# Performance work log

Measured on AMD Instinct MI355X. Metric: run time of the kernel, lower is better.

The kernel has to match this reference:

```python
import jax, jax.numpy as jnp
import numpy as np

B, S, D_IN, D, H = 2, 2048, 512, 1024, 16
HD = D // H


def _linear_params(key, d_in, d_out):
    kw, kb = jax.random.split(key)
    bound = 1.0 / np.sqrt(d_in)
    W = jax.random.uniform(kw, (d_in, d_out), jnp.float32, -bound, bound)
    b = jax.random.uniform(kb, (d_out,), jnp.float32, -bound, bound)
    return W, b


def setup_inputs() -> dict:
    key = jax.random.key(0)
    keys = jax.random.split(key, 8)
    x = jax.random.normal(keys[0], (B, S, D_IN), jnp.float32)
    We, be = _linear_params(keys[1], D_IN, D)
    Wq, bq = _linear_params(keys[2], D, D)
    Wk, bk = _linear_params(keys[3], D, D)
    Wv, bv = _linear_params(keys[4], D, D)
    W0, b0 = _linear_params(keys[5], D, D)
    W1, b1 = _linear_params(keys[6], D, D)
    W2, b2 = _linear_params(keys[7], D, D)
    return {"x": x, "We": We, "be": be, "Wq": Wq, "bq": bq, "Wk": Wk, "bk": bk,
            "Wv": Wv, "bv": bv, "W0": W0, "b0": b0, "W1": W1, "b1": b1, "W2": W2, "b2": b2}


def reference(x, We, be, Wq, bq, Wk, bk, Wv, bv, W0, b0, W1, b1, W2, b2):
    # embedding
    e = x @ We + be                                   # [B,S,D]
    q = (e @ Wq + bq).reshape(B, S, H, HD)            # [B,S,H,hd]
    k = (e @ Wk + bk).reshape(B, S, H, HD)
    v = (e @ Wv + bv).reshape(B, S, H, HD)
    scale = 1.0 / jnp.sqrt(jnp.float32(HD))
    scores = jnp.einsum('bqhd,bkhd->bhqk', q, k) * scale
    attn = jax.nn.softmax(scores, axis=-1)            # [B,H,S,S]
    ctx = jnp.einsum('bhqk,bkhd->bqhd', attn, v).reshape(B, S, D)
    mha = e + (ctx @ W0 + b0)                         # residual
    ffn = jax.nn.relu(mha @ W1 + b1) @ W2 + b2
    return mha + ffn
```

## Files before the change

### kernel.cpp

```cpp
#include <hip/hip_runtime.h>

typedef unsigned short u16;
typedef __bf16 bf16x8 __attribute__((ext_vector_type(8)));
typedef float f32x4 __attribute__((ext_vector_type(4)));

__device__ __forceinline__ float bf2f(u16 u) {
  return __builtin_bit_cast(float, (unsigned)u << 16);
}
__device__ __forceinline__ u16 f2bf(float f) {
  unsigned u = __builtin_bit_cast(unsigned, f);
  u += 0x7FFFu + ((u >> 16) & 1u);
  return (u16)(u >> 16);
}
__device__ __forceinline__ unsigned pk2(float a, float b) {
  return (unsigned)f2bf(a) | ((unsigned)f2bf(b) << 16);
}
__device__ __forceinline__ unsigned pk2t(float a, float b) {
  return __builtin_amdgcn_perm(__builtin_bit_cast(unsigned, b),
                               __builtin_bit_cast(unsigned, a), 0x07060302u);
}
__device__ __forceinline__ f32x4 mfma16(bf16x8 a, bf16x8 b, f32x4 c) {
  return __builtin_amdgcn_mfma_f32_16x16x32_bf16(a, b, c, 0, 0, 0);
}
__device__ __forceinline__ void async_cp16(const u16* g, u16* l) {
  __builtin_amdgcn_global_load_lds((const __attribute__((address_space(1))) void*)g,
                                   (__attribute__((address_space(3))) void*)l, 16, 0, 0);
}
#define S_BARRIER() asm volatile("s_barrier" ::: "memory")

#define TSP 72
__global__ __launch_bounds__(256) void prep_fused(
    const float* __restrict__ We, const float* __restrict__ Wq,
    const float* __restrict__ Wk, const float* __restrict__ Wv,
    const float* __restrict__ W0, const float* __restrict__ W1,
    const float* __restrict__ W2, const float* __restrict__ x,
    const float* __restrict__ bq, const float* __restrict__ bk,
    const float* __restrict__ bv, u16* Wet, u16* qkvWt, u16* W0t, u16* W1t,
    u16* W2t, u16* xb, float* biasqkv) {
  const int z = blockIdx.z;
  const int tid = threadIdx.x;
  if (z >= 7) {
    if (z == 15) {
      int i = (blockIdx.y * 16 + blockIdx.x) * 256 + tid;
      if (i < 3072)
        biasqkv[i] = i < 1024 ? bq[i] : (i < 2048 ? bk[i - 1024] : bv[i - 2048]);
      return;
    }
    int blin = (z - 7) * 256 + blockIdx.y * 16 + blockIdx.x;
    int idx = (blin * 256 + tid) * 4;
    float4 f = *(const float4*)&x[idx];
    ushort4 o;
    o.x = f2bf(f.x); o.y = f2bf(f.y); o.z = f2bf(f.z); o.w = f2bf(f.w);
    *(ushort4*)&xb[idx] = o;
    return;
  }
  const float* in;
  u16* out;
  int out_rs = 1024;
  if (z == 0) { if (blockIdx.y >= 8) return; in = We; out = Wet; out_rs = 512; }
  else if (z == 1) { in = Wq; out = qkvWt; }
  else if (z == 2) { in = Wk; out = qkvWt + 1048576; }
  else if (z == 3) { in = Wv; out = qkvWt + 2097152; }
  else if (z == 4) { in = W0; out = W0t; }
  else if (z == 5) { in = W1; out = W1t; }
  else { in = W2; out = W2t; }
  __shared__ alignas(16) u16 T[64][TSP];
  const int r0 = blockIdx.y * 64, c0 = blockIdx.x * 64;
#pragma unroll
  for (int it = 0; it < 4; ++it) {
    int vi = it * 256 + tid;
    int i = vi >> 4, j4 = (vi & 15) * 4;
    float4 f = *(const float4*)&in[(size_t)(r0 + i) * 1024 + c0 + j4];
    T[i][j4 + 0] = f2bf(f.x);
    T[i][j4 + 1] = f2bf(f.y);
    T[i][j4 + 2] = f2bf(f.z);
    T[i][j4 + 3] = f2bf(f.w);
  }
  __syncthreads();
#pragma unroll
  for (int it = 0; it < 2; ++it) {
    int vi = it * 256 + tid;
    int i = vi >> 3, j8 = (vi & 7) * 8;
    bf16x8 v;
#pragma unroll
    for (int u = 0; u < 8; ++u) ((u16*)&v)[u] = T[j8 + u][i];
    *(bf16x8*)&out[(size_t)(c0 + i) * out_rs + r0 + j8] = v;
  }
}

template <int TM, int TN>
__global__ __launch_bounds__(256, (TM == 128 && TN == 128) ? 2
                                  : (TM == 128)            ? 3
                                                           : 5) void gemm_mfma(
    const u16* __restrict__ A, const u16* __restrict__ Bt,
    const float* __restrict__ bias, const u16* __restrict__ res,
    void* __restrict__ Cout, int M, int N, int K, int relu, int f32out) {
  constexpr int MT = TM / 32;
  constexpr int NT = TN / 32;
  constexpr int AI = TM / 32;
  constexpr int BI = TN / 32;
  __shared__ alignas(16) u16 As[2][TM * 64];
  __shared__ alignas(16) u16 Bs[2][TN * 64];
  const int tid = threadIdx.x;
  const int wave = tid >> 6, lane = tid & 63;
  const int quad = lane >> 4, l16 = lane & 15;
  const int ib = blockIdx.x;
  int by, bx;
  if constexpr (TM == 128) { by = (ib & 7) * 4 + ((ib >> 3) & 3); bx = ib >> 5; }
  else { by = (ib & 7) * 8 + ((ib >> 3) & 7); bx = ib >> 6; }
  const int m0 = by * TM, n0 = bx * TN;
  const int wm = (wave & 1) * (TM / 2), wn = (wave >> 1) * (TN / 2);

  f32x4 acc[MT][NT];
#pragma unroll
  for (int i = 0; i < MT; ++i)
#pragma unroll
    for (int j = 0; j < NT; ++j) acc[i][j] = (f32x4){0.f, 0.f, 0.f, 0.f};

  const int srow = lane >> 3;
  const int schunk = (lane & 7) ^ (srow & 7);
  const u16* Ag = A + (size_t)(m0 + wave * (TM / 4) + srow) * K + schunk * 8;
  const u16* Bg = Bt + (size_t)(n0 + wave * (TN / 4) + srow) * K + schunk * 8;
  u16* AsW0 = &As[0][wave * (TM / 4) * 64];
  u16* BsW0 = &Bs[0][wave * (TN / 4) * 64];
  u16* AsW1 = &As[1][wave * (TM / 4) * 64];
  u16* BsW1 = &Bs[1][wave * (TN / 4) * 64];

#define GEMM_ISSUE(ab, bb, k)                                     \
  {                                                               \
    _Pragma("unroll") for (int i = 0; i < AI; ++i)                \
        async_cp16(Ag + (k) + (size_t)i * 8 * K, (ab) + i * 512); \
    _Pragma("unroll") for (int i = 0; i < BI; ++i)                \
        async_cp16(Bg + (k) + (size_t)i * 8 * K, (bb) + i * 512); \
  }

  GEMM_ISSUE(AsW0, BsW0, 0);
  const int T = K >> 6;
  const int swz = (l16 & 7);
  for (int t = 0; t < T; ++t) {
    const int cb = t & 1;
    S_BARRIER();
    const int kn = (t + 1 < T) ? ((t + 1) << 6) : 0;
    if (cb == 0) GEMM_ISSUE(AsW1, BsW1, kn) else GEMM_ISSUE(AsW0, BsW0, kn);
    if constexpr (AI + BI == 8)
      asm volatile("s_waitcnt vmcnt(8)" ::: "memory");
    else if constexpr (AI + BI == 6)
      asm volatile("s_waitcnt vmcnt(6)" ::: "memory");
    else
      asm volatile("s_waitcnt vmcnt(4)" ::: "memory");
    S_BARRIER();
#pragma unroll
    for (int kk = 0; kk < 2; ++kk) {
      bf16x8 af[MT], bfr[NT];
#pragma unroll
      for (int mt = 0; mt < MT; ++mt)
        af[mt] = *(const bf16x8*)&As[cb][(wm + mt * 16 + l16) * 64 +
                                        ((kk * 4 + quad) ^ swz) * 8];
#pragma unroll
      for (int nt = 0; nt < NT; ++nt)
        bfr[nt] = *(const bf16x8*)&Bs[cb][(wn + nt * 16 + l16) * 64 +
                                          ((kk * 4 + quad) ^ swz) * 8];
#pragma unroll
      for (int mt = 0; mt < MT; ++mt)
#pragma unroll
        for (int nt = 0; nt < NT; ++nt)
          acc[mt][nt] = mfma16(af[mt], bfr[nt], acc[mt][nt]);
    }
  }
  asm volatile("s_waitcnt vmcnt(0)" ::: "memory");

#pragma unroll
  for (int nt = 0; nt < NT; ++nt) {
    int col = n0 + wn + nt * 16 + l16;
    float bv = bias[col];
#pragma unroll
    for (int mt = 0; mt < MT; ++mt) {
#pragma unroll
      for (int r = 0; r < 4; ++r) {
        int row = m0 + wm + mt * 16 + quad * 4 + r;
        float v = acc[mt][nt][r] + bv;
        if (res) v += bf2f(res[(size_t)row * N + col]);
        if (relu) v = fmaxf(v, 0.f);
        if (f32out)
          ((float*)Cout)[(size_t)row * N + col] = v;
        else
          ((u16*)Cout)[(size_t)row * N + col] = f2bf(v);
      }
    }
  }
}

__global__ __launch_bounds__(256, 2) void attn_kernel(
    const u16* __restrict__ QKV, const u16* __restrict__ Vt,
    u16* __restrict__ O) {
  __shared__ alignas(16) u16 Ks[2][64 * 64];
  __shared__ alignas(16) u16 Vs[2][64 * 64];
  __shared__ alignas(16) u16 Ps[4][32 * 64];
  const int tid = threadIdx.x;
  const int wave = tid >> 6, lane = tid & 63;
  const int quad = lane >> 4, l16 = lane & 15;
  const int ib = blockIdx.x;
  const int bh = ib & 31, b = bh >> 4, h = bh & 15;
  const int q0 = (ib >> 5) * 128 + wave * 32;

  bf16x8 qf[2][2];
#pragma unroll
  for (int qt = 0; qt < 2; ++qt) {
    const size_t qoff = (size_t)(b * 2048 + q0 + qt * 16 + l16) * 3072 + h * 64;
#pragma unroll
    for (int kk = 0; kk < 2; ++kk) {
      bf16x8 raw = *(const bf16x8*)&QKV[qoff + kk * 32 + quad * 8];
#pragma unroll
      for (int u = 0; u < 8; ++u)
        ((u16*)&raw)[u] = f2bf(0.125f * bf2f(((u16*)&raw)[u]));
      qf[qt][kk] = raw;
    }
  }
  bf16x8 ones;
#pragma unroll
  for (int u = 0; u < 8; ++u) ((u16*)&ones)[u] = 0x3F80;

  f32x4 o[4][2];
  f32x4 l_acc[2] = {(f32x4){0.f, 0.f, 0.f, 0.f}, (f32x4){0.f, 0.f, 0.f, 0.f}};
#pragma unroll
  for (int mt = 0; mt < 4; ++mt)
#pragma unroll
    for (int qt = 0; qt < 2; ++qt) o[mt][qt] = (f32x4){0.f, 0.f, 0.f, 0.f};

  const int srow = lane >> 3;
  const int schunk = (lane & 7) ^ (srow & 7);
  const u16* Kg = QKV + (size_t)(b * 2048 + wave * 16 + srow) * 3072 + 1024 +
                  h * 64 + schunk * 8;
  const u16* Vg = Vt + (size_t)((b * 16 + h) * 64 + wave * 16 + srow) * 2048 +
                  schunk * 8;
  u16* KsW0 = &Ks[0][(wave * 16) * 64];
  u16* VsW0 = &Vs[0][(wave * 16) * 64];
  u16* KsW1 = &Ks[1][(wave * 16) * 64];
  u16* VsW1 = &Vs[1][(wave * 16) * 64];

#define ATTN_ISSUE(kb, vb, kt)                                \
  {                                                           \
    async_cp16(Kg + (size_t)(kt) * 3072, (kb));               \
    async_cp16(Kg + (size_t)((kt) + 8) * 3072, (kb) + 512);   \
    async_cp16(Vg + (kt), (vb));                              \
    async_cp16(Vg + (kt) + (size_t)8 * 2048, (vb) + 512);     \
  }

  ATTN_ISSUE(KsW0, VsW0, 0);
  const int swz = (l16 & 7);
  u16* PsW = &Ps[wave][0];
  for (int t = 0; t < 32; ++t) {
    const int cb = t & 1;
    S_BARRIER();
    const int ktn = (t + 1 < 32) ? ((t + 1) * 64) : 0;
    if (cb == 0) ATTN_ISSUE(KsW1, VsW1, ktn) else ATTN_ISSUE(KsW0, VsW0, ktn);
    asm volatile("s_waitcnt vmcnt(4)" ::: "memory");
    S_BARRIER();

    f32x4 st[4][2];
#pragma unroll
    for (int km = 0; km < 4; ++km)
#pragma unroll
      for (int qt = 0; qt < 2; ++qt) st[km][qt] = (f32x4){0.f, 0.f, 0.f, 0.f};
    __builtin_amdgcn_s_setprio(1);
#pragma unroll
    for (int kk = 0; kk < 2; ++kk)
#pragma unroll
      for (int km = 0; km < 4; ++km) {
        bf16x8 kf = *(const bf16x8*)&Ks[cb][(km * 16 + l16) * 64 +
                                           ((kk * 4 + quad) ^ swz) * 8];
        st[km][0] = mfma16(kf, qf[0][kk], st[km][0]);
        st[km][1] = mfma16(kf, qf[1][kk], st[km][1]);
      }
    __builtin_amdgcn_s_setprio(0);

#pragma unroll
    for (int qt = 0; qt < 2; ++qt)
#pragma unroll
      for (int km = 0; km < 4; ++km) {
        float e0 = __expf(st[km][qt][0]), e1 = __expf(st[km][qt][1]);
        float e2 = __expf(st[km][qt][2]), e3 = __expf(st[km][qt][3]);
        uint2 pk;
        pk.x = pk2t(e0, e1);
        pk.y = pk2t(e2, e3);
        *(uint2*)&PsW[(qt * 16 + l16) * 64 +
                      ((km * 2 + (quad >> 1)) ^ swz) * 8 + (quad & 1) * 4] = pk;
      }
    asm volatile("s_waitcnt lgkmcnt(0)" ::: "memory");

    __builtin_amdgcn_s_setprio(1);
#pragma unroll
    for (int kk2 = 0; kk2 < 2; ++kk2) {
      bf16x8 pf0 =
          *(const bf16x8*)&PsW[l16 * 64 + ((kk2 * 4 + quad) ^ swz) * 8];
      bf16x8 pf1 = *(const bf16x8*)&PsW[(16 + l16) * 64 +
                                        ((kk2 * 4 + quad) ^ swz) * 8];
      l_acc[0] = mfma16(ones, pf0, l_acc[0]);
      l_acc[1] = mfma16(ones, pf1, l_acc[1]);
#pragma unroll
      for (int mt = 0; mt < 4; ++mt) {
        bf16x8 vf = *(const bf16x8*)&Vs[cb][(mt * 16 + l16) * 64 +
                                           ((kk2 * 4 + quad) ^ swz) * 8];
        o[mt][0] = mfma16(vf, pf0, o[mt][0]);
        o[mt][1] = mfma16(vf, pf1, o[mt][1]);
      }
    }
    __builtin_amdgcn_s_setprio(0);
  }
  asm volatile("s_waitcnt vmcnt(0)" ::: "memory");

#pragma unroll
  for (int qt = 0; qt < 2; ++qt) {
    float inv = 1.f / l_acc[qt][0];
    size_t base = (size_t)(b * 2048 + q0 + qt * 16 + l16) * 1024 + h * 64;
#pragma unroll
    for (int mt = 0; mt < 4; ++mt) {
      uint2 pk;
      pk.x = pk2(o[mt][qt][0] * inv, o[mt][qt][1] * inv);
      pk.y = pk2(o[mt][qt][2] * inv, o[mt][qt][3] * inv);
      *(uint2*)&O[base + mt * 16 + quad * 4] = pk;
    }
  }
}

__global__ __launch_bounds__(256) void transpose_v(const u16* __restrict__ QKV,
                                                   u16* __restrict__ vt) {
  const int bh = blockIdx.y;
  const int b = bh >> 4, h = bh & 15;
  const int s0 = blockIdx.x * 64;
  const u16* in = QKV + (size_t)b * 2048 * 3072 + 2048 + h * 64;
  u16* out = vt + (size_t)bh * 131072;
  __shared__ alignas(16) u16 T[64][TSP];
  const int tid = threadIdx.x;
#pragma unroll
  for (int it = 0; it < 2; ++it) {
    int vi = it * 256 + tid;
    int i = vi >> 3, j8 = (vi & 7) * 8;
    *(bf16x8*)&T[i][j8] = *(const bf16x8*)&in[(size_t)(s0 + i) * 3072 + j8];
  }
  __syncthreads();
#pragma unroll
  for (int it = 0; it < 2; ++it) {
    int vi = it * 256 + tid;
    int i = vi >> 3, j8 = (vi & 7) * 8;
    bf16x8 vv;
#pragma unroll
    for (int u = 0; u < 8; ++u) ((u16*)&vv)[u] = T[j8 + u][i];
    *(bf16x8*)&out[(size_t)i * 2048 + s0 + j8] = vv;
  }
}

extern "C" void kernel_launch(void* const* d_in, const int* in_sizes, int n_in,
                              void* d_out, int out_size, void* d_ws,
                              size_t ws_size, hipStream_t stream) {
  const float* x = (const float*)d_in[0];
  const float* We = (const float*)d_in[1];
  const float* be = (const float*)d_in[2];
  const float* Wq = (const float*)d_in[3];
  const float* bq = (const float*)d_in[4];
  const float* Wk = (const float*)d_in[5];
  const float* bk = (const float*)d_in[6];
  const float* Wv = (const float*)d_in[7];
  const float* bv = (const float*)d_in[8];
  const float* W0 = (const float*)d_in[9];
  const float* b0 = (const float*)d_in[10];
  const float* W1 = (const float*)d_in[11];
  const float* b1 = (const float*)d_in[12];
  const float* W2 = (const float*)d_in[13];
  const float* b2 = (const float*)d_in[14];

  u16* ws = (u16*)d_ws;
  u16* xb = ws;
  u16* Wet = xb + 2097152;
  u16* qkvWt = Wet + 524288;
  u16* ctx = ws;
  u16* W0t = qkvWt + 3145728;
  u16* W1t = W0t + 1048576;
  u16* W2t = W1t + 1048576;
  float* biasqkv = (float*)(W2t + 1048576);
  u16* e = W2t + 1048576 + 6144;
  u16* qkv = e + 4194304;
  u16* vtb = qkv + 12582912;
  u16* mha = qkv;
  u16* h1 = e;

  prep_fused<<<dim3(16, 16, 16), 256, 0, stream>>>(
      We, Wq, Wk, Wv, W0, W1, W2, x, bq, bk, bv, Wet, qkvWt, W0t, W1t, W2t,
      xb, biasqkv);

  gemm_mfma<64, 64><<<1024, 256, 0, stream>>>(xb, Wet, be, nullptr, e, 4096,
                                              1024, 512, 0, 0);
  gemm_mfma<128, 128><<<768, 256, 0, stream>>>(e, qkvWt, biasqkv, nullptr, qkv,
                                               4096, 3072, 1024, 0, 0);
  transpose_v<<<dim3(32, 32), 256, 0, stream>>>(qkv, vtb);
  attn_kernel<<<512, 256, 0, stream>>>(qkv, vtb, ctx);
  gemm_mfma<64, 64><<<1024, 256, 0, stream>>>(ctx, W0t, b0, e, mha, 4096, 1024,
                                              1024, 0, 0);
  gemm_mfma<64, 64><<<1024, 256, 0, stream>>>(mha, W1t, b1, nullptr, h1, 4096,
                                              1024, 1024, 1, 0);
  gemm_mfma<64, 64><<<1024, 256, 0, stream>>>(h1, W2t, b2, mha, d_out, 4096,
                                              1024, 1024, 0, 1);
}
```

Baseline: 261.8 us.

## Fold embedding weights into QKV projection to shrink the QKV GEMM's K dimension

Precomputes the combined weight Wc = We·Wqkv (a 3072x512 GEMM over the weights) and the combined bias bc = be·Wqkv + bqkv, so QKV is computed directly from x with K=512 instead of from e with K=1024. This roughly halves the FLOPs of the largest projection, at the cost of an extra small weight GEMM, a bias kernel and a bf16 copy of We written during prep. The extra bf16 rounding of the combined weights slightly changes numerics. The QKV GEMM now uses 128x64 tiles, and the 8-load wait path is removed.

Result: slower. 283.9 us (+8.4%).

```diff
diff --git a/kernel.cpp b/kernel.cpp
--- a/kernel.cpp
+++ b/kernel.cpp
@@ -36,7 +36,7 @@
     const float* __restrict__ W2, const float* __restrict__ x,
     const float* __restrict__ bq, const float* __restrict__ bk,
     const float* __restrict__ bv, u16* Wet, u16* qkvWt, u16* W0t, u16* W1t,
-    u16* W2t, u16* xb, float* biasqkv) {
+    u16* W2t, u16* xb, float* biasqkv, u16* Web) {
   const int z = blockIdx.z;
   const int tid = threadIdx.x;
   if (z >= 7) {
@@ -71,10 +71,14 @@
     int vi = it * 256 + tid;
     int i = vi >> 4, j4 = (vi & 15) * 4;
     float4 f = *(const float4*)&in[(size_t)(r0 + i) * 1024 + c0 + j4];
-    T[i][j4 + 0] = f2bf(f.x);
-    T[i][j4 + 1] = f2bf(f.y);
-    T[i][j4 + 2] = f2bf(f.z);
-    T[i][j4 + 3] = f2bf(f.w);
+    ushort4 o;
+    o.x = f2bf(f.x); o.y = f2bf(f.y); o.z = f2bf(f.z); o.w = f2bf(f.w);
+    T[i][j4 + 0] = o.x;
+    T[i][j4 + 1] = o.y;
+    T[i][j4 + 2] = o.z;
+    T[i][j4 + 3] = o.w;
+    if (z == 0)
+      *(ushort4*)&Web[(size_t)(r0 + i) * 1024 + c0 + j4] = o;
   }
   __syncthreads();
 #pragma unroll
@@ -88,10 +92,24 @@
   }
 }
 
-template <int TM, int TN>
-__global__ __launch_bounds__(256, (TM == 128 && TN == 128) ? 2
-                                  : (TM == 128)            ? 3
-                                                           : 5) void gemm_mfma(
+__global__ __launch_bounds__(256) void bc_kernel(const u16* __restrict__ qkvWt,
+                                                 const float* __restrict__ be,
+                                                 const float* __restrict__ biasqkv,
+                                                 float* __restrict__ bc) {
+  int n = blockIdx.x * 256 + threadIdx.x;
+  if (n >= 3072) return;
+  const u16* row = qkvWt + (size_t)n * 1024;
+  float s = biasqkv[n];
+  for (int j = 0; j < 1024; j += 8) {
+    bf16x8 v = *(const bf16x8*)&row[j];
+#pragma unroll
+    for (int u = 0; u < 8; ++u) s += be[j + u] * bf2f(((u16*)&v)[u]);
+  }
+  bc[n] = s;
+}
+
+template <int TM, int TN, bool SWZ = true>
+__global__ __launch_bounds__(256, (TM == 128) ? 3 : 5) void gemm_mfma(
     const u16* __restrict__ A, const u16* __restrict__ Bt,
     const float* __restrict__ bias, const u16* __restrict__ res,
     void* __restrict__ Cout, int M, int N, int K, int relu, int f32out) {
@@ -106,7 +124,8 @@
   const int quad = lane >> 4, l16 = lane & 15;
   const int ib = blockIdx.x;
   int by, bx;
-  if constexpr (TM == 128) { by = (ib & 7) * 4 + ((ib >> 3) & 3); bx = ib >> 5; }
+  if constexpr (!SWZ) { const int yb = M / TM; by = ib % yb; bx = ib / yb; }
+  else if constexpr (TM == 128) { by = (ib & 7) * 4 + ((ib >> 3) & 3); bx = ib >> 5; }
   else { by = (ib & 7) * 8 + ((ib >> 3) & 7); bx = ib >> 6; }
   const int m0 = by * TM, n0 = bx * TN;
   const int wm = (wave & 1) * (TM / 2), wn = (wave >> 1) * (TN / 2);
@@ -142,9 +161,7 @@
     S_BARRIER();
     const int kn = (t + 1 < T) ? ((t + 1) << 6) : 0;
     if (cb == 0) GEMM_ISSUE(AsW1, BsW1, kn) else GEMM_ISSUE(AsW0, BsW0, kn);
-    if constexpr (AI + BI == 8)
-      asm volatile("s_waitcnt vmcnt(8)" ::: "memory");
-    else if constexpr (AI + BI == 6)
+    if constexpr (AI + BI == 6)
       asm volatile("s_waitcnt vmcnt(6)" ::: "memory");
     else
       asm volatile("s_waitcnt vmcnt(4)" ::: "memory");
@@ -172,7 +189,7 @@
 #pragma unroll
   for (int nt = 0; nt < NT; ++nt) {
     int col = n0 + wn + nt * 16 + l16;
-    float bv = bias[col];
+    float bv = bias ? bias[col] : 0.f;
 #pragma unroll
     for (int mt = 0; mt < MT; ++mt) {
 #pragma unroll
@@ -383,15 +400,21 @@
   u16* vtb = qkv + 12582912;
   u16* mha = qkv;
   u16* h1 = e;
+  u16* Web = e;
+  u16* Wct = vtb;
+  float* bc = (float*)(vtb + 4194304);
 
   prep_fused<<<dim3(16, 16, 16), 256, 0, stream>>>(
       We, Wq, Wk, Wv, W0, W1, W2, x, bq, bk, bv, Wet, qkvWt, W0t, W1t, W2t,
-      xb, biasqkv);
-
+      xb, biasqkv, Web);
+
+  bc_kernel<<<12, 256, 0, stream>>>(qkvWt, be, biasqkv, bc);
+  gemm_mfma<64, 64, false><<<384, 256, 0, stream>>>(
+      qkvWt, Web, nullptr, nullptr, Wct, 3072, 512, 1024, 0, 0);
+  gemm_mfma<128, 64><<<1536, 256, 0, stream>>>(xb, Wct, bc, nullptr, qkv, 4096,
+                                               3072, 512, 0, 0);
   gemm_mfma<64, 64><<<1024, 256, 0, stream>>>(xb, Wet, be, nullptr, e, 4096,
                                               1024, 512, 0, 0);
-  gemm_mfma<128, 128><<<768, 256, 0, stream>>>(e, qkvWt, biasqkv, nullptr, qkv,
-                                               4096, 3072, 1024, 0, 0);
   transpose_v<<<dim3(32, 32), 256, 0, stream>>>(qkv, vtb);
   attn_kernel<<<512, 256, 0, stream>>>(qkv, vtb, ctx);
   gemm_mfma<64, 64><<<1024, 256, 0, stream>>>(ctx, W0t, b0, e, mha, 4096, 1024,
```

## Fuse V transpose into QKV GEMM epilogue and switch to 128x64 tiles

Applied to the files above, without the earlier changes.

The QKV projection GEMM now writes the V third of its output directly in transposed per-head layout, so the separate transpose_v kernel launch and its extra read/write of V are removed. The QKV GEMM tile changes from 128x128 to 128x64 with 1536 blocks, which gives more blocks but less reuse per block. The transposed stores are 4-element strided writes along the sequence dimension, which may coalesce poorly.

Result: faster. 249.2 us, median of 4 (-4.8%).

```diff
diff --git a/kernel.cpp b/kernel.cpp
--- a/kernel.cpp
+++ b/kernel.cpp
@@ -88,13 +88,12 @@
   }
 }
 
-template <int TM, int TN>
-__global__ __launch_bounds__(256, (TM == 128 && TN == 128) ? 2
-                                  : (TM == 128)            ? 3
-                                                           : 5) void gemm_mfma(
+template <int TM, int TN, bool VT = false>
+__global__ __launch_bounds__(256, (TM == 128) ? 3 : 5) void gemm_mfma(
     const u16* __restrict__ A, const u16* __restrict__ Bt,
     const float* __restrict__ bias, const u16* __restrict__ res,
-    void* __restrict__ Cout, int M, int N, int K, int relu, int f32out) {
+    void* __restrict__ Cout, int M, int N, int K, int relu, int f32out,
+    u16* __restrict__ vt) {
   constexpr int MT = TM / 32;
   constexpr int NT = TN / 32;
   constexpr int AI = TM / 32;
@@ -142,9 +141,7 @@
     S_BARRIER();
     const int kn = (t + 1 < T) ? ((t + 1) << 6) : 0;
     if (cb == 0) GEMM_ISSUE(AsW1, BsW1, kn) else GEMM_ISSUE(AsW0, BsW0, kn);
-    if constexpr (AI + BI == 8)
-      asm volatile("s_waitcnt vmcnt(8)" ::: "memory");
-    else if constexpr (AI + BI == 6)
+    if constexpr (AI + BI == 6)
       asm volatile("s_waitcnt vmcnt(6)" ::: "memory");
     else
       asm volatile("s_waitcnt vmcnt(4)" ::: "memory");
@@ -172,19 +169,33 @@
 #pragma unroll
   for (int nt = 0; nt < NT; ++nt) {
     int col = n0 + wn + nt * 16 + l16;
-    float bv = bias[col];
+    float bv = bias ? bias[col] : 0.f;
 #pragma unroll
     for (int mt = 0; mt < MT; ++mt) {
+      int row0 = m0 + wm + mt * 16 + quad * 4;
+      float vv[4];
 #pragma unroll
       for (int r = 0; r < 4; ++r) {
-        int row = m0 + wm + mt * 16 + quad * 4 + r;
         float v = acc[mt][nt][r] + bv;
-        if (res) v += bf2f(res[(size_t)row * N + col]);
+        if (res) v += bf2f(res[(size_t)(row0 + r) * N + col]);
         if (relu) v = fmaxf(v, 0.f);
-        if (f32out)
-          ((float*)Cout)[(size_t)row * N + col] = v;
-        else
-          ((u16*)Cout)[(size_t)row * N + col] = f2bf(v);
+        vv[r] = v;
+      }
+      if (VT && col >= 2048) {
+        int bb = row0 >> 11, ss = row0 & 2047;
+        int hh = (col >> 6) & 15, dd = col & 63;
+        uint2 pk;
+        pk.x = pk2(vv[0], vv[1]);
+        pk.y = pk2(vv[2], vv[3]);
+        *(uint2*)&vt[(((size_t)(bb * 16 + hh) * 64 + dd) << 11) + ss] = pk;
+      } else {
+#pragma unroll
+        for (int r = 0; r < 4; ++r) {
+          if (f32out)
+            ((float*)Cout)[(size_t)(row0 + r) * N + col] = vv[r];
+          else
+            ((u16*)Cout)[(size_t)(row0 + r) * N + col] = f2bf(vv[r]);
+        }
       }
     }
   }
@@ -320,33 +331,6 @@
       pk.y = pk2(o[mt][qt][2] * inv, o[mt][qt][3] * inv);
       *(uint2*)&O[base + mt * 16 + quad * 4] = pk;
     }
-  }
-}
-
-__global__ __launch_bounds__(256) void transpose_v(const u16* __restrict__ QKV,
-                                                   u16* __restrict__ vt) {
-  const int bh = blockIdx.y;
-  const int b = bh >> 4, h = bh & 15;
-  const int s0 = blockIdx.x * 64;
-  const u16* in = QKV + (size_t)b * 2048 * 3072 + 2048 + h * 64;
-  u16* out = vt + (size_t)bh * 131072;
-  __shared__ alignas(16) u16 T[64][TSP];
-  const int tid = threadIdx.x;
-#pragma unroll
-  for (int it = 0; it < 2; ++it) {
-    int vi = it * 256 + tid;
-    int i = vi >> 3, j8 = (vi & 7) * 8;
-    *(bf16x8*)&T[i][j8] = *(const bf16x8*)&in[(size_t)(s0 + i) * 3072 + j8];
-  }
-  __syncthreads();
-#pragma unroll
-  for (int it = 0; it < 2; ++it) {
-    int vi = it * 256 + tid;
-    int i = vi >> 3, j8 = (vi & 7) * 8;
-    bf16x8 vv;
-#pragma unroll
-    for (int u = 0; u < 8; ++u) ((u16*)&vv)[u] = T[j8 + u][i];
-    *(bf16x8*)&out[(size_t)i * 2048 + s0 + j8] = vv;
   }
 }
 
@@ -389,15 +373,14 @@
       xb, biasqkv);
 
   gemm_mfma<64, 64><<<1024, 256, 0, stream>>>(xb, Wet, be, nullptr, e, 4096,
-                                              1024, 512, 0, 0);
-  gemm_mfma<128, 128><<<768, 256, 0, stream>>>(e, qkvWt, biasqkv, nullptr, qkv,
-                                               4096, 3072, 1024, 0, 0);
-  transpose_v<<<dim3(32, 32), 256, 0, stream>>>(qkv, vtb);
+                                              1024, 512, 0, 0, nullptr);
+  gemm_mfma<128, 64, true><<<1536, 256, 0, stream>>>(
+      e, qkvWt, biasqkv, nullptr, qkv, 4096, 3072, 1024, 0, 0, vtb);
   attn_kernel<<<512, 256, 0, stream>>>(qkv, vtb, ctx);
   gemm_mfma<64, 64><<<1024, 256, 0, stream>>>(ctx, W0t, b0, e, mha, 4096, 1024,
-                                              1024, 0, 0);
+                                              1024, 0, 0, nullptr);
   gemm_mfma<64, 64><<<1024, 256, 0, stream>>>(mha, W1t, b1, nullptr, h1, 4096,
-                                              1024, 1024, 1, 0);
+                                              1024, 1024, 1, 0, nullptr);
   gemm_mfma<64, 64><<<1024, 256, 0, stream>>>(h1, W2t, b2, mha, d_out, 4096,
-                                              1024, 1024, 0, 1);
-}
+                                              1024, 1024, 0, 1, nullptr);
+}
```
